# Kernel optimization log

Hardware: AMD Instinct MI355X
Metric: run time of the kernel (lower is better)

The kernel has to match this reference:

```python
import jax, jax.numpy as jnp
import numpy as np

B, CIN, COUT, S1, S2, M1, M2 = 16, 64, 64, 128, 128, 16, 16


def _cas(L, dtype):
    # Hartley 'cas' matrix: cos(2*pi*k*k'/L) + sin(2*pi*k*k'/L), symmetric LxL
    k = jnp.arange(L, dtype=dtype)
    ang = (2.0 * jnp.pi / L) * (k[:, None] * k[None, :])
    return jnp.cos(ang) + jnp.sin(ang)


def dht2(x):
    # x: [B, C, M, N] -> dense 2D discrete Hartley transform via matmuls
    M, N = x.shape[-2], x.shape[-1]
    cas_row = _cas(M, x.dtype)
    cas_col = _cas(N, x.dtype)
    # torch: matmul(x, cas_col.T) then matmul(cas_row.T, .)
    y = jnp.einsum('bimn,gn->bimg', x, cas_col)
    return jnp.einsum('mf,bimn->bifn', cas_row, y)


def idht2(x):
    return dht2(x) / (x.shape[-2] * x.shape[-1])


def _neg_freq(a):
    # roll(flip(a, [-1,-2]), (1,1), [-1,-2])
    return jnp.roll(jnp.flip(a, axis=(-2, -1)), shift=(1, 1), axis=(-2, -1))


def compl_mul2d(x1, x2):
    x1n = _neg_freq(x1)
    x2n = _neg_freq(x2)
    e = lambda a, b: jnp.einsum('bixy,ioxy->boxy', a, b)
    return 0.5 * (e(x1, x2) - e(x1n, x2n) + e(x1, x2n) + e(x1n, x2))


def setup_inputs() -> dict:
    key = jax.random.key(0)
    k1, k2, k3 = jax.random.split(key, 3)
    scale = 1.0 / (CIN * COUT)
    x = jax.random.normal(k1, (B, CIN, S1, S2), dtype=jnp.float32)
    weights1 = scale * jax.random.uniform(k2, (CIN, COUT, M1, M2), dtype=jnp.float32)
    weights2 = scale * jax.random.uniform(k3, (CIN, COUT, M1, M2), dtype=jnp.float32)
    return {'x': x, 'weights1': weights1, 'weights2': weights2}


def reference(x, weights1, weights2):
    m1, m2 = weights1.shape[2], weights1.shape[3]
    b, cout = x.shape[0], weights1.shape[1]
    s1, s2 = x.shape[-2], x.shape[-1]

    cos_part = dht2(x)
    sin_part = dht2(jnp.flip(x, axis=(-2, -1)))
    # torch.angle(complex(cos, sin)) == atan2(sin, cos)
    phase = jnp.arctan2(sin_part, cos_part)

    out_dht = jnp.zeros((b, cout, s1, s2), dtype=x.dtype)
    out_dht = out_dht.at[:, :, :m1, :m2].set(
        compl_mul2d(cos_part[:, :, :m1, :m2], weights1))
    out_dht = out_dht.at[:, :, -m1:, :m2].set(
        compl_mul2d(cos_part[:, :, -m1:, :m2], weights2))

    y = idht2(out_dht)
    return y * jnp.cos(phase)
```

## Files before the change

kernel.cpp:

```cpp
#include <hip/hip_runtime.h>

typedef _Float16 f16;
typedef f16 f16x8 __attribute__((ext_vector_type(8)));
typedef float f32x4 __attribute__((ext_vector_type(4)));

#define LSCALE 2048.0f
#define LINV   4.8828125e-4f
#define XS 136

#define MFMA(A,B,C) __builtin_amdgcn_mfma_f32_16x16x32_f16(A, B, C, 0, 0, 0)

__device__ __forceinline__ int frag_slot(int row, int k) {
    return ((((row >> 4) * 4 + (k >> 5)) * 64) + ((k >> 3) & 3) * 16 + (row & 15)) * 8 + (k & 7);
}

__global__ void k_cas(float* __restrict__ casf,
                      f16* __restrict__ FAh, f16* __restrict__ FAl,
                      f16* __restrict__ FVh, f16* __restrict__ FVl) {
    int f = blockIdx.x, m = threadIdx.x;
    const float SC = (float)(6.283185307179586 / 128.0);
    float ang = SC * (float)(f * m);
    double a = (double)ang;
    float v = (float)cos(a) + (float)sin(a);
    casf[f * 128 + m] = v;
    f16 h = (f16)v;
    f16 lo = (f16)((v - (float)h) * LSCALE);
    int sA = frag_slot(f, m);
    FAh[sA] = h;
    FAl[sA] = lo;
    int sV = frag_slot(f, 127 - m);
    FVh[sV] = h;
    FVl[sV] = lo;
}

__global__ __launch_bounds__(1024) void k_dht(
    const float* __restrict__ xg,
    const f16* __restrict__ FAh, const f16* __restrict__ FAl,
    const f16* __restrict__ FVh, const f16* __restrict__ FVl,
    float* __restrict__ outbuf,
    float* __restrict__ cp1, float* __restrict__ cp2)
{
    __shared__ __align__(16) char smem[143360];
    f16* Xh  = (f16*)smem;
    f16* Xl  = (f16*)(smem + 35840);
    f16* W1h = (f16*)smem;
    f16* W1l = (f16*)(smem + 35840);
    f16* W2h = (f16*)(smem + 71680);
    f16* W2l = (f16*)(smem + 107520);

    const int img = blockIdx.x;
    const float* X = xg + (size_t)img * 16384;
    const int t = threadIdx.x;
    const int lane = t & 63;
    const int wv = t >> 6;
    const int l15 = lane & 15;
    const int a4 = lane >> 4;

    #pragma unroll
    for (int it = 0; it < 4; ++it) {
        int i = it * 1024 + t;
        int r = i >> 5, c0 = (i & 31) * 4;
        float4 xv = *(const float4*)&X[r * 128 + c0];
        const float* xp = (const float*)&xv;
        #pragma unroll
        for (int j = 0; j < 4; ++j) {
            f16 h = (f16)xp[j];
            Xh[r * XS + c0 + j] = h;
            Xl[r * XS + c0 + j] = (f16)((xp[j] - (float)h) * LSCALE);
        }
    }
    __syncthreads();

    const int gw = wv & 7;
    const int mh = (wv >> 3) * 4;
    f32x4 w1hi[4], w1lo[4], w2hi[4], w2lo[4];
    #pragma unroll
    for (int i = 0; i < 4; ++i) {
        w1hi[i] = (f32x4){0.f,0.f,0.f,0.f}; w1lo[i] = (f32x4){0.f,0.f,0.f,0.f};
        w2hi[i] = (f32x4){0.f,0.f,0.f,0.f}; w2lo[i] = (f32x4){0.f,0.f,0.f,0.f};
    }
    {
        #pragma unroll 1
        for (int ks = 0; ks < 4; ++ks) {
            const int toff = ((gw * 4 + ks) * 64 + lane) * 8;
            f16x8 tah = *(const f16x8*)&FAh[toff];
            f16x8 tal = *(const f16x8*)&FAl[toff];
            f16x8 tvh = *(const f16x8*)&FVh[toff];
            f16x8 tvl = *(const f16x8*)&FVl[toff];
            #pragma unroll
            for (int mi = 0; mi < 4; ++mi) {
                const int base = (16 * (mh + mi) + l15) * XS + ks * 32 + 8 * a4;
                f16x8 xh = *(const f16x8*)&Xh[base];
                f16x8 xl = *(const f16x8*)&Xl[base];
                w1hi[mi] = MFMA(tah, xh, w1hi[mi]);
                w1lo[mi] = MFMA(tal, xh, w1lo[mi]);
                w1lo[mi] = MFMA(tah, xl, w1lo[mi]);
                w2hi[mi] = MFMA(tvh, xh, w2hi[mi]);
                w2lo[mi] = MFMA(tvl, xh, w2lo[mi]);
                w2lo[mi] = MFMA(tvh, xl, w2lo[mi]);
            }
        }
    }
    __syncthreads();

    {
        const int g = 16 * gw + 4 * a4;
        #pragma unroll
        for (int mi = 0; mi < 4; ++mi) {
            const int m = 16 * (mh + mi) + l15;
            #pragma unroll
            for (int r = 0; r < 4; ++r) {
                float v1 = w1hi[mi][r] + LINV * w1lo[mi][r];
                f16 h1 = (f16)v1;
                float v2 = w2hi[mi][r] + LINV * w2lo[mi][r];
                f16 h2 = (f16)v2;
                W2h[(g + r) * XS + m] = h2;
                W2l[(g + r) * XS + m] = (f16)((v2 - (float)h2) * LSCALE);
                W1h[(g + r) * XS + m] = h1;
                W1l[(g + r) * XS + m] = (f16)((v1 - (float)h1) * LSCALE);
            }
        }
    }
    __syncthreads();

    const int ft = wv >> 1;
    const int gh = wv & 1;
    f32x4 chi[4], clo[4], shi[4], slo[4];
    #pragma unroll
    for (int i = 0; i < 4; ++i) {
        chi[i] = (f32x4){0.f,0.f,0.f,0.f}; clo[i] = (f32x4){0.f,0.f,0.f,0.f};
        shi[i] = (f32x4){0.f,0.f,0.f,0.f}; slo[i] = (f32x4){0.f,0.f,0.f,0.f};
    }
    {
        #pragma unroll 1
        for (int ks = 0; ks < 4; ++ks) {
            const int toff = ((ft * 4 + ks) * 64 + lane) * 8;
            f16x8 tah = *(const f16x8*)&FAh[toff];
            f16x8 tal = *(const f16x8*)&FAl[toff];
            f16x8 tvh = *(const f16x8*)&FVh[toff];
            f16x8 tvl = *(const f16x8*)&FVl[toff];
            #pragma unroll
            for (int gi = 0; gi < 4; ++gi) {
                const int gt = 4 * gh + gi;
                const int base = (16 * gt + l15) * XS + ks * 32 + 8 * a4;
                f16x8 u1h = *(const f16x8*)&W1h[base];
                f16x8 u1l = *(const f16x8*)&W1l[base];
                f16x8 u2h = *(const f16x8*)&W2h[base];
                f16x8 u2l = *(const f16x8*)&W2l[base];
                chi[gi] = MFMA(tah, u1h, chi[gi]);
                clo[gi] = MFMA(tal, u1h, clo[gi]);
                clo[gi] = MFMA(tah, u1l, clo[gi]);
                shi[gi] = MFMA(tvh, u2h, shi[gi]);
                slo[gi] = MFMA(tvl, u2h, slo[gi]);
                slo[gi] = MFMA(tvh, u2l, slo[gi]);
            }
        }
    }

    f16* cph = (f16*)(outbuf + (size_t)img * 16384);
    #pragma unroll
    for (int gi = 0; gi < 4; ++gi) {
        const int g = 16 * (4 * gh + gi) + l15;
        #pragma unroll
        for (int r = 0; r < 4; ++r) {
            const int f = 16 * ft + 4 * a4 + r;
            float Cv = chi[gi][r] + LINV * clo[gi][r];
            float Sv = shi[gi][r] + LINV * slo[gi][r];
            float d = Cv * Cv + Sv * Sv;
            float cp = (d > 0.f) ? Cv * rsqrtf(d) : 1.0f;
            cph[f * 128 + g] = (f16)cp;
            if (gh == 0 && gi == 0) {
                if (ft == 0)      cp1[img * 256 + f * 16 + l15] = Cv;
                else if (ft == 7) cp2[img * 256 + (f - 112) * 16 + l15] = Cv;
            }
        }
    }
}

__global__ __launch_bounds__(256) void k_corner(
    const float* __restrict__ cp1, const float* __restrict__ cp2,
    const float* __restrict__ w1,  const float* __restrict__ w2,
    float* __restrict__ od1, float* __restrict__ od2)
{
    const int c = blockIdx.y;
    const float* cp = c ? cp2 : cp1;
    const float* w  = c ? w2  : w1;
    float* od       = c ? od2 : od1;
    const int b = blockIdx.x >> 6, o = blockIdx.x & 63;
    const int t = threadIdx.x;
    const int xx = t >> 4, yy = t & 15;
    const int nx = (16 - xx) & 15, ny = (16 - yy) & 15;

    float acc = 0.f;
    #pragma unroll 4
    for (int i = 0; i < 64; ++i) {
        float A  = cp[((b * 64 + i) * 16 + xx) * 16 + yy];
        float An = cp[((b * 64 + i) * 16 + nx) * 16 + ny];
        float W  = w[((i * 64 + o) * 16 + xx) * 16 + yy];
        float Wn = w[((i * 64 + o) * 16 + nx) * 16 + ny];
        acc += A * (W + Wn) + An * (W - Wn);
    }
    od[((b * 64 + o) * 16 + xx) * 16 + yy] = 0.5f * acc;
}

__global__ __launch_bounds__(256) void k_inv(
    const float* __restrict__ od1, const float* __restrict__ od2,
    const float* __restrict__ cas,
    float* __restrict__ out)
{
    __shared__ float odS[32 * 16];
    __shared__ float casF[128 * 33];
    __shared__ float Rs[128 * 17];
    __shared__ float casG[16 * 128];
    __shared__ __align__(16) unsigned short cphS[16384];

    const int img = blockIdx.x;
    const int t = threadIdx.x;

    const uint4* cp16 = (const uint4*)(out + (size_t)img * 16384);
    #pragma unroll
    for (int k = 0; k < 8; ++k) {
        int i = k * 256 + t;
        ((uint4*)cphS)[i] = cp16[i];
    }

    odS[t]       = od1[img * 256 + t];
    odS[256 + t] = od2[img * 256 + t];
    #pragma unroll
    for (int k = 0; k < 16; ++k) {
        int idx = t + k * 256;
        int s = idx >> 5, j = idx & 31;
        int f = (j < 16) ? j : (96 + j);
        casF[s * 33 + j] = cas[s * 128 + f];
    }
    #pragma unroll
    for (int k = 0; k < 8; ++k) {
        int idx = t + k * 256;
        casG[idx] = cas[idx];
    }
    __syncthreads();

    {
        const int s1 = t >> 1, gb = (t & 1) * 8;
        float acc[8];
        #pragma unroll
        for (int l = 0; l < 8; ++l) acc[l] = 0.f;
        #pragma unroll 4
        for (int j = 0; j < 32; ++j) {
            float cf = casF[s1 * 33 + j];
            #pragma unroll
            for (int l = 0; l < 8; ++l)
                acc[l] = fmaf(cf, odS[j * 16 + gb + l], acc[l]);
        }
        #pragma unroll
        for (int l = 0; l < 8; ++l) Rs[s1 * 17 + gb + l] = acc[l];
    }
    __syncthreads();

    const float inv = 1.0f / 16384.0f;
    const int grp = t >> 5, lane = t & 31;
    const int s2 = lane * 4;
    for (int r = 0; r < 16; ++r) {
        const int s1 = grp * 16 + r;
        float4 acc = {0.f, 0.f, 0.f, 0.f};
        #pragma unroll
        for (int g = 0; g < 16; ++g) {
            float rv = Rs[s1 * 17 + g];
            float4 c4 = *(const float4*)&casG[g * 128 + s2];
            acc.x = fmaf(rv, c4.x, acc.x);
            acc.y = fmaf(rv, c4.y, acc.y);
            acc.z = fmaf(rv, c4.z, acc.z);
            acc.w = fmaf(rv, c4.w, acc.w);
        }
        const f16* ph = (const f16*)cphS + s1 * 128 + s2;
        size_t idx = (size_t)img * 16384 + (size_t)s1 * 128 + s2;
        float4 res;
        res.x = acc.x * inv * (float)ph[0];
        res.y = acc.y * inv * (float)ph[1];
        res.z = acc.z * inv * (float)ph[2];
        res.w = acc.w * inv * (float)ph[3];
        *(float4*)&out[idx] = res;
    }
}

extern "C" void kernel_launch(void* const* d_in, const int* in_sizes, int n_in,
                              void* d_out, int out_size, void* d_ws, size_t ws_size,
                              hipStream_t stream) {
    (void)in_sizes; (void)n_in; (void)out_size; (void)ws_size;
    const float* x  = (const float*)d_in[0];
    const float* w1 = (const float*)d_in[1];
    const float* w2 = (const float*)d_in[2];
    float* out = (float*)d_out;
    float* ws  = (float*)d_ws;

    float* casf = ws;
    f16* FAh = (f16*)(ws + 16384);
    f16* FAl = FAh + 16384;
    f16* FVh = FAl + 16384;
    f16* FVl = FVh + 16384;
    float* cp1 = (float*)(FVl + 16384);
    float* cp2 = cp1 + 262144;
    float* od1 = cp2 + 262144;
    float* od2 = od1 + 262144;

    k_cas<<<dim3(128), dim3(128), 0, stream>>>(casf, FAh, FAl, FVh, FVl);
    k_dht<<<dim3(1024), dim3(1024), 0, stream>>>(x, FAh, FAl, FVh, FVl, out, cp1, cp2);
    k_corner<<<dim3(1024, 2), dim3(256), 0, stream>>>(cp1, cp2, w1, w2, od1, od2);
    k_inv<<<dim3(1024), dim3(256), 0, stream>>>(od1, od2, casf, out);
}
```

Baseline: 148.5 us.

## Fuse corner spectral multiply into inverse kernel and vectorize hi/lo stores

```diff
diff --git a/kernel.cpp b/kernel.cpp
--- a/kernel.cpp
+++ b/kernel.cpp
@@ -1,6 +1,7 @@
 #include <hip/hip_runtime.h>
 
 typedef _Float16 f16;
+typedef f16 f16x4 __attribute__((ext_vector_type(4)));
 typedef f16 f16x8 __attribute__((ext_vector_type(8)));
 typedef float f32x4 __attribute__((ext_vector_type(4)));
 
@@ -62,12 +63,15 @@
         int r = i >> 5, c0 = (i & 31) * 4;
         float4 xv = *(const float4*)&X[r * 128 + c0];
         const float* xp = (const float*)&xv;
+        f16x4 hv, lv;
         #pragma unroll
         for (int j = 0; j < 4; ++j) {
             f16 h = (f16)xp[j];
-            Xh[r * XS + c0 + j] = h;
-            Xl[r * XS + c0 + j] = (f16)((xp[j] - (float)h) * LSCALE);
-        }
+            hv[j] = h;
+            lv[j] = (f16)((xp[j] - (float)h) * LSCALE);
+        }
+        *(f16x4*)&Xh[r * XS + c0] = hv;
+        *(f16x4*)&Xl[r * XS + c0] = lv;
     }
     __syncthreads();
 
@@ -177,34 +181,9 @@
     }
 }
 
-__global__ __launch_bounds__(256) void k_corner(
+__global__ __launch_bounds__(256) void k_inv(
     const float* __restrict__ cp1, const float* __restrict__ cp2,
     const float* __restrict__ w1,  const float* __restrict__ w2,
-    float* __restrict__ od1, float* __restrict__ od2)
-{
-    const int c = blockIdx.y;
-    const float* cp = c ? cp2 : cp1;
-    const float* w  = c ? w2  : w1;
-    float* od       = c ? od2 : od1;
-    const int b = blockIdx.x >> 6, o = blockIdx.x & 63;
-    const int t = threadIdx.x;
-    const int xx = t >> 4, yy = t & 15;
-    const int nx = (16 - xx) & 15, ny = (16 - yy) & 15;
-
-    float acc = 0.f;
-    #pragma unroll 4
-    for (int i = 0; i < 64; ++i) {
-        float A  = cp[((b * 64 + i) * 16 + xx) * 16 + yy];
-        float An = cp[((b * 64 + i) * 16 + nx) * 16 + ny];
-        float W  = w[((i * 64 + o) * 16 + xx) * 16 + yy];
-        float Wn = w[((i * 64 + o) * 16 + nx) * 16 + ny];
-        acc += A * (W + Wn) + An * (W - Wn);
-    }
-    od[((b * 64 + o) * 16 + xx) * 16 + yy] = 0.5f * acc;
-}
-
-__global__ __launch_bounds__(256) void k_inv(
-    const float* __restrict__ od1, const float* __restrict__ od2,
     const float* __restrict__ cas,
     float* __restrict__ out)
 {
@@ -215,6 +194,7 @@
     __shared__ __align__(16) unsigned short cphS[16384];
 
     const int img = blockIdx.x;
+    const int b = img >> 6, o = img & 63;
     const int t = threadIdx.x;
 
     const uint4* cp16 = (const uint4*)(out + (size_t)img * 16384);
@@ -224,8 +204,30 @@
         ((uint4*)cphS)[i] = cp16[i];
     }
 
-    odS[t]       = od1[img * 256 + t];
-    odS[256 + t] = od2[img * 256 + t];
+    {
+        const int xx = t >> 4, yy = t & 15;
+        const int nx = (16 - xx) & 15, ny = (16 - yy) & 15;
+        const int pf = xx * 16 + yy, pn = nx * 16 + ny;
+        float acc1 = 0.f, acc2 = 0.f;
+        #pragma unroll 4
+        for (int i = 0; i < 64; ++i) {
+            const int cb = (b * 64 + i) * 256;
+            const int wb = (i * 64 + o) * 256;
+            float A1  = cp1[cb + pf];
+            float A1n = cp1[cb + pn];
+            float W1v = w1[wb + pf];
+            float W1n = w1[wb + pn];
+            acc1 += A1 * (W1v + W1n) + A1n * (W1v - W1n);
+            float A2  = cp2[cb + pf];
+            float A2n = cp2[cb + pn];
+            float W2v = w2[wb + pf];
+            float W2n = w2[wb + pn];
+            acc2 += A2 * (W2v + W2n) + A2n * (W2v - W2n);
+        }
+        odS[pf]       = 0.5f * acc1;
+        odS[256 + pf] = 0.5f * acc2;
+    }
+
     #pragma unroll
     for (int k = 0; k < 16; ++k) {
         int idx = t + k * 256;
@@ -300,11 +302,8 @@
     f16* FVl = FVh + 16384;
     float* cp1 = (float*)(FVl + 16384);
     float* cp2 = cp1 + 262144;
-    float* od1 = cp2 + 262144;
-    float* od2 = od1 + 262144;
 
     k_cas<<<dim3(128), dim3(128), 0, stream>>>(casf, FAh, FAl, FVh, FVl);
     k_dht<<<dim3(1024), dim3(1024), 0, stream>>>(x, FAh, FAl, FVh, FVl, out, cp1, cp2);
-    k_corner<<<dim3(1024, 2), dim3(256), 0, stream>>>(cp1, cp2, w1, w2, od1, od2);
-    k_inv<<<dim3(1024), dim3(256), 0, stream>>>(od1, od2, casf, out);
-}
+    k_inv<<<dim3(1024), dim3(256), 0, stream>>>(cp1, cp2, w1, w2, casf, out);
+}
```

New measurement: 139.7 us. -5.9%, faster.
